# Kernel tuning notes

Measured on AMD Instinct MI355X. Metric: run time of the kernel, lower is better.

Reference implementation:

```python
import jax, jax.numpy as jnp
import numpy as np

BN_EPS = 1e-3  # keras BatchNormalization default epsilon


def conv1x1(x, w):
    # x: [N,C,H,W], w: [O,C] (1x1 conv, no bias)
    return jnp.einsum('nchw,oc->nohw', x, w)


def bn(x, gamma, beta, mean, var):
    # inference-mode batchnorm over channel axis 1
    scale = gamma / jnp.sqrt(var + BN_EPS)
    shift = beta - mean * scale
    return x * scale[None, :, None, None] + shift[None, :, None, None]


def fourier_unit(x, w, gamma, beta, mean, var):
    # x: [N,C,H,W] NCHW. 1D rfft over W (matches tf.signal.rfft), normalized by sqrt(W).
    N, C, H, W = x.shape
    norm = jnp.sqrt(jnp.float32(W))
    f = jnp.fft.rfft(x / norm, axis=-1)          # [N,C,H,Wf] complex64, Wf=W//2+1
    Wf = f.shape[-1]
    # interleave re/im per channel: [N,C,2,H,Wf] -> [N,2C,H,Wf]
    ff = jnp.stack([jnp.real(f), jnp.imag(f)], axis=2).reshape(N, 2 * C, H, Wf)
    y = jax.nn.relu(bn(conv1x1(ff, w), gamma, beta, mean, var))  # [N,2C,H,Wf]
    Co = y.shape[1] // 2
    y = y.reshape(N, Co, 2, H, Wf)
    c = jax.lax.complex(y[:, :, 0], y[:, :, 1])
    return jnp.fft.irfft(c, n=W, axis=-1) * norm  # [N,Co,H,W]


def setup_inputs() -> dict:
    key = jax.random.key(0)
    ks = jax.random.split(key, 20)
    N, H, W, Cin = 8, 128, 128, 256
    fmaps = 256
    half = fmaps // 2  # 128

    def nrm(k, shape, s=0.05):
        return jax.random.normal(k, shape, dtype=jnp.float32) * s

    def bn_params(k, c):
        k1, k2, k3, k4 = jax.random.split(k, 4)
        gamma = jax.random.uniform(k1, (c,), dtype=jnp.float32) + 0.5
        beta = nrm(k2, (c,), 0.1)
        mean = nrm(k3, (c,), 0.1)
        var = jax.random.uniform(k4, (c,), dtype=jnp.float32) + 0.5
        return gamma, beta, mean, var

    x = jax.random.normal(ks[0], (N, H, W, Cin), dtype=jnp.float32)
    w1 = nrm(ks[1], (half, Cin))
    g1, b1, m1, v1 = bn_params(ks[2], half)
    fu_w = nrm(ks[3], (2 * half, 2 * half))
    fu_g, fu_b, fu_m, fu_v = bn_params(ks[4], 2 * half)
    lfu_w = nrm(ks[5], (2 * half, 2 * half))
    lfu_g, lfu_b, lfu_m, lfu_v = bn_params(ks[6], 2 * half)
    w2 = nrm(ks[7], (fmaps, half))
    return {
        'x': x, 'w1': w1, 'g1': g1, 'b1': b1, 'm1': m1, 'v1': v1,
        'fu_w': fu_w, 'fu_g': fu_g, 'fu_b': fu_b, 'fu_m': fu_m, 'fu_v': fu_v,
        'lfu_w': lfu_w, 'lfu_g': lfu_g, 'lfu_b': lfu_b, 'lfu_m': lfu_m, 'lfu_v': lfu_v,
        'w2': w2,
    }


def reference(x, w1, g1, b1, m1, v1,
              fu_w, fu_g, fu_b, fu_m, fu_v,
              lfu_w, lfu_g, lfu_b, lfu_m, lfu_v,
              w2):
    # NHWC -> NCHW (stride=1, no downsample)
    x = jnp.transpose(x, (0, 3, 1, 2))
    x = jax.nn.relu(bn(conv1x1(x, w1), g1, b1, m1, v1))  # [N,half,H,W]
    out = fourier_unit(x, fu_w, fu_g, fu_b, fu_m, fu_v)
    # local fourier unit: take first C//4 channels, fold 2x2 spatial patches into channels
    C = x.shape[1]
    xs = x[:, :C // 4]
    xs = jnp.concatenate(jnp.split(xs, 2, axis=2), axis=1)  # split H
    xs = jnp.concatenate(jnp.split(xs, 2, axis=3), axis=1)  # split W -> [N,C,H/2,W/2]
    xs = fourier_unit(xs, lfu_w, lfu_g, lfu_b, lfu_m, lfu_v)
    xs = jnp.tile(xs, (1, 1, 2, 2))  # back to [N,C,H,W]
    out = conv1x1(x + out + xs, w2)  # [N,fmaps,H,W]
    return jnp.transpose(out, (0, 2, 3, 1))  # NCHW -> NHWC
```

## Files before the change

kernel.cpp:

```cpp
#include <hip/hip_runtime.h>
#include <math.h>

typedef __attribute__((ext_vector_type(8))) short short8;
typedef __attribute__((ext_vector_type(4))) float f32x4;

#define SW7b(r) (((r) & 7) << 4)
#define SW3b(r) (((r) & 3) << 4)

static __device__ __forceinline__ unsigned short f2b(float f){
  unsigned u = __float_as_uint(f);
  u = (u + 0x7FFFu + ((u >> 16) & 1u)) >> 16;
  return (unsigned short)u;
}
static __device__ __forceinline__ float b2f(unsigned short u){
  return __uint_as_float(((unsigned)u) << 16);
}
static __device__ __forceinline__ void gl16(const void* g, void* l) {
  __builtin_amdgcn_global_load_lds(
      (const __attribute__((address_space(1))) void*)g,
      (__attribute__((address_space(3))) void*)l, 16, 0, 0);
}

__global__ void k_wt(const float* __restrict__ w1, const float* __restrict__ fu_w,
                     const float* __restrict__ lfu_w, const float* __restrict__ w2,
                     const float* __restrict__ g1, const float* __restrict__ b1,
                     const float* __restrict__ m1, const float* __restrict__ v1,
                     const float* __restrict__ fg, const float* __restrict__ fb,
                     const float* __restrict__ fm, const float* __restrict__ fv,
                     const float* __restrict__ lg_, const float* __restrict__ lb_,
                     const float* __restrict__ lm_, const float* __restrict__ lv_,
                     unsigned short* __restrict__ w1b, unsigned short* __restrict__ fuwb,
                     unsigned short* __restrict__ lfuwb, unsigned short* __restrict__ w2b,
                     unsigned short* __restrict__ DFTf, unsigned short* __restrict__ IDFTf,
                     unsigned short* __restrict__ DFTl, unsigned short* __restrict__ IDFTl,
                     float* __restrict__ sc1, float* __restrict__ sh1,
                     float* __restrict__ scF, float* __restrict__ shF,
                     float* __restrict__ scL, float* __restrict__ shL) {
  int t = blockIdx.x * 256 + threadIdx.x;
  const float TPI = 6.283185307179586f;
  if (t < 32768) {
    { int co = t >> 8, k = t & 255; w1b[co * 256 + (k ^ ((co & 7) << 3))] = f2b(w1[t]); }
    { int co = t >> 7, k = t & 127; w2b[co * 128 + (k ^ ((co & 7) << 3))] = f2b(w2[t]); }
  }
  if (t < 65536) {
    int co = t >> 8, k = t & 255;
    fuwb[co * 256 + (k ^ ((co & 7) << 3))] = f2b(fu_w[t]);
    lfuwb[co * 256 + (k ^ ((co & 7) << 3))] = f2b(lfu_w[t]);
  }
  if (t < 18432) {
    int m = t >> 7, w = t & 127; float v = 0.f;
    if (m < 130) {
      int wf = m >> 1; int ph = (wf * w) & 127;
      float ang = TPI * (float)ph / 128.f;
      v = ((m & 1) ? -sinf(ang) : cosf(ang)) * 0.08838834764831845f;
    }
    DFTf[m * 128 + (w ^ ((m & 7) << 3))] = f2b(v);
  }
  if (t < 20480) {
    int m = t / 160, k2 = t % 160; float v = 0.f;
    if (k2 < 130) {
      int wf = k2 >> 1; float a = (wf == 0 || wf == 64) ? 1.f : 2.f;
      int ph = (wf * m) & 127;
      float ang = TPI * (float)ph / 128.f;
      v = ((k2 & 1) ? -a * sinf(ang) : a * cosf(ang)) * 0.08838834764831845f;
    }
    IDFTf[m * 160 + (k2 ^ ((m & 3) << 3))] = f2b(v);
  }
  if (t < 5120) {
    int m = t >> 6, w = t & 63; float v = 0.f;
    if (m < 66) {
      int wf = m >> 1; int ph = (wf * w) & 63;
      float ang = TPI * (float)ph / 64.f;
      v = ((m & 1) ? -sinf(ang) : cosf(ang)) * 0.125f;
    }
    DFTl[m * 64 + (w ^ ((m & 7) << 3))] = f2b(v);
  }
  if (t < 6144) {
    int m = t / 96, k2 = t % 96; float v = 0.f;
    if (k2 < 66) {
      int wf = k2 >> 1; float a = (wf == 0 || wf == 32) ? 1.f : 2.f;
      int ph = (wf * m) & 63;
      float ang = TPI * (float)ph / 64.f;
      v = ((k2 & 1) ? -a * sinf(ang) : a * cosf(ang)) * 0.125f;
    }
    IDFTl[m * 96 + (k2 ^ ((m & 3) << 3))] = f2b(v);
  }
  if (t < 128) { float s = g1[t] * rsqrtf(v1[t] + 1e-3f); sc1[t] = s; sh1[t] = b1[t] - m1[t] * s; }
  if (t < 256) { float s = fg[t] * rsqrtf(fv[t] + 1e-3f); scF[t] = s; shF[t] = fb[t] - fm[t] * s; }
  if (t < 256) { float s = lg_[t] * rsqrtf(lv_[t] + 1e-3f); scL[t] = s; shL[t] = lb_[t] - lm_[t] * s; }
}

__global__ __launch_bounds__(256) void k_conv1(const unsigned short* __restrict__ A,
                                               const float* __restrict__ x,
                                               unsigned short* __restrict__ X1c,
                                               const float* __restrict__ scp,
                                               const float* __restrict__ shp) {
  __shared__ __align__(16) char A_s[128 * 512];
  __shared__ __align__(16) char B_s[128 * 128];
  int t = threadIdx.x; int wid = t >> 6, l = t & 63;
  int wm = wid >> 1, wn = wid & 1;
  int m0 = wm * 64; int lr = l & 15, lg = l >> 4;
  size_t nh = blockIdx.x;
  const char* Ab = (const char*)A;
  const char* xrow = (const char*)(x + nh * 128 * 256);
  #pragma unroll
  for (int i = 0; i < 16; i++) { int g = i * 256 + t; gl16(Ab + g * 16, A_s + g * 16); }
  f32x4 acc[4][4];
  #pragma unroll
  for (int mt = 0; mt < 4; mt++)
    #pragma unroll
    for (int nt = 0; nt < 4; nt++) acc[mt][nt] = (f32x4){0.f, 0.f, 0.f, 0.f};
  for (int kk = 0; kk < 256; kk += 32) {
    #pragma unroll
    for (int i = 0; i < 4; i++) {
      int g = i * 256 + t; int w = g >> 3, o = g & 7;
      gl16(xrow + (size_t)w * 1024 + kk * 4 + ((o * 16) ^ SW7b(w)), B_s + g * 16);
    }
    __syncthreads();
    short8 af[4], bf[4];
    #pragma unroll
    for (int mt = 0; mt < 4; mt++) {
      int m = m0 + 16 * mt + lr;
      af[mt] = *(const short8*)(A_s + m * 512 + ((kk * 2 + lg * 16) ^ SW7b(m)));
    }
    #pragma unroll
    for (int nt = 0; nt < 4; nt++) {
      int w = wn * 64 + 16 * nt + lr;
      float4 f0 = *(const float4*)(B_s + w * 128 + ((lg * 32) ^ SW7b(w)));
      float4 f1 = *(const float4*)(B_s + w * 128 + ((lg * 32 + 16) ^ SW7b(w)));
      short8 bb;
      bb[0] = (short)f2b(f0.x); bb[1] = (short)f2b(f0.y);
      bb[2] = (short)f2b(f0.z); bb[3] = (short)f2b(f0.w);
      bb[4] = (short)f2b(f1.x); bb[5] = (short)f2b(f1.y);
      bb[6] = (short)f2b(f1.z); bb[7] = (short)f2b(f1.w);
      bf[nt] = bb;
    }
    #pragma unroll
    for (int mt = 0; mt < 4; mt++)
      #pragma unroll
      for (int nt = 0; nt < 4; nt++)
        acc[mt][nt] = __builtin_amdgcn_mfma_f32_16x16x32_bf16(af[mt], bf[nt], acc[mt][nt], 0, 0, 0);
    __syncthreads();
  }
  char* xout = (char*)X1c + nh * 32768;
  #pragma unroll
  for (int nt = 0; nt < 4; nt++) {
    int w = wn * 64 + 16 * nt + lr;
    #pragma unroll
    for (int mt = 0; mt < 4; mt++) {
      int rb = m0 + 16 * mt + lg * 4;
      float4 s4 = *(const float4*)&scp[rb];
      float4 h4 = *(const float4*)&shp[rb];
      f32x4 v = acc[mt][nt];
      *(unsigned short*)(xout + (rb + 0) * 256 + ((w * 2) ^ SW7b(rb + 0))) = f2b(fmaxf(v[0] * s4.x + h4.x, 0.f));
      *(unsigned short*)(xout + (rb + 1) * 256 + ((w * 2) ^ SW7b(rb + 1))) = f2b(fmaxf(v[1] * s4.y + h4.y, 0.f));
      *(unsigned short*)(xout + (rb + 2) * 256 + ((w * 2) ^ SW7b(rb + 2))) = f2b(fmaxf(v[2] * s4.z + h4.z, 0.f));
      *(unsigned short*)(xout + (rb + 3) * 256 + ((w * 2) ^ SW7b(rb + 3))) = f2b(fmaxf(v[3] * s4.w + h4.w, 0.f));
    }
  }
}

__global__ __launch_bounds__(256) void k_lfu(const unsigned short* __restrict__ DFTm,
                                             const unsigned short* __restrict__ lfuw,
                                             const unsigned short* __restrict__ IDFTm,
                                             const unsigned short* __restrict__ X1c,
                                             const float* __restrict__ scp,
                                             const float* __restrict__ shp,
                                             unsigned short* __restrict__ XSO) {
  __shared__ __align__(16) char SH[81920];
  char* M   = SH;
  char* Xs  = SH + 16384;
  char* FFl = SH + 32768;
  char* Yl  = SH + 57344;
  int t = threadIdx.x, wid = t >> 6, l = t & 63, lr = l & 15, lg = l >> 4;
  int b = blockIdx.x; int n = b >> 6, h2 = b & 63;
  {
    const char* src = (const char*)DFTm;
    #pragma unroll
    for (int i = 0; i < 3; i++) { int g = i * 256 + t; if (g < 640) gl16(src + g * 16, M + g * 16); }
    #pragma unroll
    for (int i = 0; i < 4; i++) {
      int g = i * 256 + t; int c2 = g >> 3, o = g & 7;
      int c0 = c2 & 31, hb = (c2 >> 5) & 1, wbq = (c2 >> 6) & 1;
      const char* s = (const char*)X1c +
          ((size_t)(n * 128 + hb * 64 + h2) * 128 + c0) * 256 + wbq * 128 + o * 16;
      gl16(s, Xs + g * 16);
    }
    #pragma unroll
    for (int i = 0; i < 8; i++) {
      int u = i * 256 + t;
      if (u < 1920) *(unsigned*)(FFl + 33 * 512 + u * 4) = 0u;
    }
  }
  __syncthreads();
  {
    f32x4 acc[5][2];
    #pragma unroll
    for (int mt = 0; mt < 5; mt++) { acc[mt][0] = (f32x4){0,0,0,0}; acc[mt][1] = (f32x4){0,0,0,0}; }
    for (int kk = 0; kk < 64; kk += 32) {
      int kb = kk * 2 + lg * 16;
      short8 bf[2];
      #pragma unroll
      for (int nt = 0; nt < 2; nt++) {
        int c2 = wid * 32 + 16 * nt + lr;
        bf[nt] = *(const short8*)(Xs + c2 * 128 + (kb ^ SW7b(c2)));
      }
      #pragma unroll
      for (int mt = 0; mt < 5; mt++) {
        int m = 16 * mt + lr;
        short8 af = *(const short8*)(M + m * 128 + (kb ^ SW7b(m)));
        #pragma unroll
        for (int nt = 0; nt < 2; nt++)
          acc[mt][nt] = __builtin_amdgcn_mfma_f32_16x16x32_bf16(af, bf[nt], acc[mt][nt], 0, 0, 0);
      }
    }
    #pragma unroll
    for (int nt = 0; nt < 2; nt++) {
      int c2 = wid * 32 + 16 * nt + lr;
      #pragma unroll
      for (int mt = 0; mt < 5; mt++) {
        int rb = 16 * mt + lg * 4;
        int wf0 = rb >> 1;
        f32x4 v = acc[mt][nt];
        if (wf0 < 33) {
          unsigned pk = (unsigned)f2b(v[0]) | ((unsigned)f2b(v[1]) << 16);
          *(unsigned*)(FFl + wf0 * 512 + ((4 * c2) ^ SW7b(wf0))) = pk;
        }
        if (wf0 + 1 < 33) {
          unsigned pk = (unsigned)f2b(v[2]) | ((unsigned)f2b(v[3]) << 16);
          *(unsigned*)(FFl + (wf0 + 1) * 512 + ((4 * c2) ^ SW7b(wf0 + 1))) = pk;
        }
      }
    }
  }
  __syncthreads();
  int wm2 = wid >> 1, wn2 = wid & 1;
  for (int ch = 0; ch < 8; ch++) {
    {
      const char* src = (const char*)lfuw + (size_t)ch * 16384;
      #pragma unroll
      for (int i = 0; i < 4; i++) { int g = i * 256 + t; gl16(src + g * 16, M + g * 16); }
    }
    __syncthreads();
    int NT = wn2 ? 1 : 2;
    f32x4 acc[2];
    acc[0] = (f32x4){0,0,0,0}; acc[1] = (f32x4){0,0,0,0};
    int lm = wm2 * 16 + lr;
    for (int kk = 0; kk < 256; kk += 32) {
      int kb = kk * 2 + lg * 16;
      short8 af = *(const short8*)(M + lm * 512 + (kb ^ SW7b(lm)));
      #pragma unroll
      for (int j = 0; j < 2; j++) {
        if (j < NT) {
          int wf = wn2 * 32 + 16 * j + lr;
          short8 bf = *(const short8*)(FFl + wf * 512 + (kb ^ SW7b(wf)));
          acc[j] = __builtin_amdgcn_mfma_f32_16x16x32_bf16(af, bf, acc[j], 0, 0, 0);
        }
      }
    }
    int co = ch * 32 + wm2 * 16 + lg * 4;
    float4 s4 = *(const float4*)&scp[co];
    float4 h4 = *(const float4*)&shp[co];
    int cc0 = co >> 1;
    #pragma unroll
    for (int j = 0; j < 2; j++) {
      if (j < NT) {
        int wf = wn2 * 32 + 16 * j + lr;
        f32x4 v = acc[j];
        float v0 = fmaxf(v[0] * s4.x + h4.x, 0.f);
        float v1 = fmaxf(v[1] * s4.y + h4.y, 0.f);
        float v2 = fmaxf(v[2] * s4.z + h4.z, 0.f);
        float v3 = fmaxf(v[3] * s4.w + h4.w, 0.f);
        unsigned p0 = (unsigned)f2b(v0) | ((unsigned)f2b(v1) << 16);
        unsigned p1 = (unsigned)f2b(v2) | ((unsigned)f2b(v3) << 16);
        *(unsigned*)(Yl + (cc0 + 0) * 192 + ((4 * wf) ^ SW3b(cc0 + 0))) = p0;
        *(unsigned*)(Yl + (cc0 + 1) * 192 + ((4 * wf) ^ SW3b(cc0 + 1))) = p1;
      }
    }
    __syncthreads();
  }
  {
    const char* src = (const char*)IDFTm;
    #pragma unroll
    for (int i = 0; i < 3; i++) { int g = i * 256 + t; gl16(src + g * 16, M + g * 16); }
  }
  __syncthreads();
  {
    f32x4 acc[8];
    #pragma unroll
    for (int nt = 0; nt < 8; nt++) acc[nt] = (f32x4){0,0,0,0};
    int w = wid * 16 + lr;
    for (int kk = 0; kk < 96; kk += 32) {
      int kb = kk * 2 + lg * 16;
      short8 af = *(const short8*)(M + w * 192 + (kb ^ SW3b(w)));
      #pragma unroll
      for (int nt = 0; nt < 8; nt++) {
        int cc = 16 * nt + lr;
        short8 bf = *(const short8*)(Yl + cc * 192 + (kb ^ SW3b(cc)));
        acc[nt] = __builtin_amdgcn_mfma_f32_16x16x32_bf16(af, bf, acc[nt], 0, 0, 0);
      }
    }
    int w0 = wid * 16 + lg * 4;
    #pragma unroll
    for (int nt = 0; nt < 8; nt++) {
      int cc = 16 * nt + lr;
      f32x4 v = acc[nt];
      ushort4 o;
      o.x = f2b(v[0]); o.y = f2b(v[1]); o.z = f2b(v[2]); o.w = f2b(v[3]);
      *(ushort4*)(XSO + (((size_t)n * 128 + cc) * 64 + h2) * 64 + w0) = o;
    }
  }
}

__global__ __launch_bounds__(1024, 4) void k_fu(const unsigned short* __restrict__ DFTm,
                                                const unsigned short* __restrict__ fuw,
                                                const unsigned short* __restrict__ IDFTm,
                                                const unsigned short* __restrict__ w2m,
                                                const unsigned short* __restrict__ X1c,
                                                const unsigned short* __restrict__ XSO,
                                                const float* __restrict__ scF,
                                                const float* __restrict__ shF,
                                                float* __restrict__ out) {
  __shared__ __align__(16) char SH[157696];
  char* M0 = SH;
  char* M1 = SH + 36864;
  char* FF = SH + 73728;
  char* Yb = SH + 114688;
  int t = threadIdx.x, wid = t >> 6, l = t & 63, lr = l & 15, lg = l >> 4;
  size_t nh = blockIdx.x;
  int n = (int)(nh >> 7), h = (int)(nh & 127);
  const char* xb = (const char*)X1c + nh * 32768;

  {
    const int nops = 36864 >> 4;
    #pragma unroll
    for (int i_ = 0; i_ < 3; i_++) {
      int g_ = i_ * 1024 + t;
      if (g_ < nops) gl16((const char*)DFTm + (size_t)g_ * 16, M0 + g_ * 16);
    }
    if (t < 1920) *(unsigned*)(FF + 65 * 512 + t * 4) = 0u;
  }
  __syncthreads();
  {
    #pragma unroll
    for (int i_ = 0; i_ < 2; i_++) {
      int g_ = i_ * 1024 + t;
      gl16((const char*)fuw + (size_t)g_ * 16, M1 + g_ * 16);
    }
    int wm1 = wid >> 3, wn1 = wid & 7;
    int c = wn1 * 16 + lr;
    short8 bf[4];
    #pragma unroll
    for (int ks = 0; ks < 4; ks++)
      bf[ks] = *(const short8*)(xb + c * 256 + ((ks * 64 + lg * 16) ^ SW7b(c)));
    f32x4 acc[5];
    #pragma unroll
    for (int mt = 0; mt < 5; mt++) acc[mt] = (f32x4){0,0,0,0};
    #pragma unroll
    for (int ks = 0; ks < 4; ks++) {
      int kb = ks * 64 + lg * 16;
      #pragma unroll
      for (int mt = 0; mt < 5; mt++) {
        int m = 16 * (wm1 * 4 + mt) + lr;
        short8 af = *(const short8*)(M0 + m * 256 + (kb ^ SW7b(m)));
        acc[mt] = __builtin_amdgcn_mfma_f32_16x16x32_bf16(af, bf[ks], acc[mt], 0, 0, 0);
      }
    }
    #pragma unroll
    for (int mt = 0; mt < 5; mt++) {
      int rb = 16 * (wm1 * 4 + mt) + lg * 4;
      int wf0 = rb >> 1;
      f32x4 v = acc[mt];
      if (wf0 < 65) {
        unsigned pk = (unsigned)f2b(v[0]) | ((unsigned)f2b(v[1]) << 16);
        *(unsigned*)(FF + wf0 * 512 + ((4 * c) ^ SW7b(wf0))) = pk;
      }
      if (wf0 + 1 < 65) {
        unsigned pk = (unsigned)f2b(v[2]) | ((unsigned)f2b(v[3]) << 16);
        *(unsigned*)(FF + (wf0 + 1) * 512 + ((4 * c) ^ SW7b(wf0 + 1))) = pk;
      }
    }
  }
  int mb2 = wid & 3, wn2 = wid >> 2;
  int mloc2 = mb2 * 16 + lr;
  #pragma unroll
  for (int ch = 0; ch < 4; ch++) {
    char* Mc = (ch & 1) ? M0 : M1;
    char* Mn = (ch & 1) ? M1 : M0;
    __syncthreads();
    if (ch < 3) {
      #pragma unroll
      for (int i_ = 0; i_ < 2; i_++) {
        int g_ = i_ * 1024 + t;
        gl16((const char*)fuw + (size_t)(ch + 1) * 32768 + (size_t)g_ * 16, Mn + g_ * 16);
      }
    } else {
      #pragma unroll
      for (int i_ = 0; i_ < 2; i_++) {
        int g_ = i_ * 1024 + t;
        if (g_ < 1280) gl16((const char*)IDFTm + (size_t)g_ * 16, Mn + g_ * 16);
      }
    }
    f32x4 acc[2];
    acc[0] = (f32x4){0,0,0,0}; acc[1] = (f32x4){0,0,0,0};
    int NJ = (wn2 == 0) ? 2 : 1;
    int j0 = wn2, j1 = 4;
    #pragma unroll
    for (int ks = 0; ks < 8; ks++) {
      int kb = ks * 64 + lg * 16;
      short8 af = *(const short8*)(Mc + mloc2 * 512 + (kb ^ SW7b(mloc2)));
      {
        int wf = j0 * 16 + lr;
        short8 b0 = *(const short8*)(FF + wf * 512 + (kb ^ SW7b(wf)));
        acc[0] = __builtin_amdgcn_mfma_f32_16x16x32_bf16(af, b0, acc[0], 0, 0, 0);
      }
      if (NJ == 2) {
        int wf = j1 * 16 + lr;
        short8 b1 = *(const short8*)(FF + wf * 512 + (kb ^ SW7b(wf)));
        acc[1] = __builtin_amdgcn_mfma_f32_16x16x32_bf16(af, b1, acc[1], 0, 0, 0);
      }
    }
    int co = ch * 64 + mb2 * 16 + lg * 4;
    float4 s4 = *(const float4*)&scF[co];
    float4 h4 = *(const float4*)&shF[co];
    int cc0 = co >> 1;
    #pragma unroll
    for (int jj = 0; jj < 2; jj++) {
      if (jj < NJ) {
        int wf = (jj == 0 ? j0 : j1) * 16 + lr;
        f32x4 v = acc[jj];
        float v0 = fmaxf(v[0] * s4.x + h4.x, 0.f);
        float v1 = fmaxf(v[1] * s4.y + h4.y, 0.f);
        float v2 = fmaxf(v[2] * s4.z + h4.z, 0.f);
        float v3 = fmaxf(v[3] * s4.w + h4.w, 0.f);
        unsigned p0 = (unsigned)f2b(v0) | ((unsigned)f2b(v1) << 16);
        unsigned p1 = (unsigned)f2b(v2) | ((unsigned)f2b(v3) << 16);
        *(unsigned*)(Yb + (size_t)(cc0 + 0) * 336 + 4 * wf) = p0;
        *(unsigned*)(Yb + (size_t)(cc0 + 1) * 336 + 4 * wf) = p1;
      }
    }
  }
  int mb3 = wid & 3, wn3 = wid >> 2;
  #pragma unroll
  for (int ck = 0; ck < 2; ck++) {
    char* Mc = ck ? M0 : M1;
    __syncthreads();
    if (ck == 0) {
      #pragma unroll
      for (int i_ = 0; i_ < 2; i_++) {
        int g_ = i_ * 1024 + t;
        if (g_ < 1280) gl16((const char*)IDFTm + 20480 + (size_t)g_ * 16, M0 + g_ * 16);
      }
    } else {
      #pragma unroll
      for (int i_ = 0; i_ < 2; i_++) {
        int g_ = i_ * 1024 + t;
        gl16((const char*)w2m + (size_t)g_ * 16, M1 + g_ * 16);
      }
    }
    int mloc = mb3 * 16 + lr;
    int w0 = ck * 64 + mb3 * 16 + lg * 4;
    ushort4 rx[2], rs[2];
    #pragma unroll
    for (int jj = 0; jj < 2; jj++) {
      int cc = (wn3 + jj * 4) * 16 + lr;
      rx[jj] = *(const ushort4*)(xb + cc * 256 + ((w0 * 2) ^ SW7b(cc)));
      rs[jj] = *(const ushort4*)(XSO + (((size_t)n * 128 + cc) * 64 + (h & 63)) * 64 + (w0 & 63));
    }
    f32x4 acc[2];
    acc[0] = (f32x4){0,0,0,0}; acc[1] = (f32x4){0,0,0,0};
    #pragma unroll
    for (int ks = 0; ks < 5; ks++) {
      int kb = ks * 64 + lg * 16;
      short8 af = *(const short8*)(Mc + mloc * 320 + (kb ^ SW3b(mloc)));
      #pragma unroll
      for (int jj = 0; jj < 2; jj++) {
        int cc = (wn3 + jj * 4) * 16 + lr;
        short8 bf = *(const short8*)(Yb + (size_t)cc * 336 + kb);
        acc[jj] = __builtin_amdgcn_mfma_f32_16x16x32_bf16(af, bf, acc[jj], 0, 0, 0);
      }
    }
    #pragma unroll
    for (int jj = 0; jj < 2; jj++) {
      int cc = (wn3 + jj * 4) * 16 + lr;
      f32x4 v = acc[jj];
      float f0 = v[0] + b2f(rx[jj].x) + b2f(rs[jj].x);
      float f1 = v[1] + b2f(rx[jj].y) + b2f(rs[jj].y);
      float f2_ = v[2] + b2f(rx[jj].z) + b2f(rs[jj].z);
      float f3 = v[3] + b2f(rx[jj].w) + b2f(rs[jj].w);
      *(unsigned short*)(FF + (w0 + 0) * 256 + ((cc * 2) ^ SW7b(w0 + 0))) = f2b(f0);
      *(unsigned short*)(FF + (w0 + 1) * 256 + ((cc * 2) ^ SW7b(w0 + 1))) = f2b(f1);
      *(unsigned short*)(FF + (w0 + 2) * 256 + ((cc * 2) ^ SW7b(w0 + 2))) = f2b(f2_);
      *(unsigned short*)(FF + (w0 + 3) * 256 + ((cc * 2) ^ SW7b(w0 + 3))) = f2b(f3);
    }
  }
  int mb4 = wid & 7, wn4 = wid >> 3;
  int mloc4 = mb4 * 16 + lr;
  #pragma unroll
  for (int ck = 0; ck < 2; ck++) {
    char* Mc = ck ? M0 : M1;
    __syncthreads();
    if (ck == 0) {
      #pragma unroll
      for (int i_ = 0; i_ < 2; i_++) {
        int g_ = i_ * 1024 + t;
        gl16((const char*)w2m + 32768 + (size_t)g_ * 16, M0 + g_ * 16);
      }
    }
    f32x4 acc[4];
    #pragma unroll
    for (int nt = 0; nt < 4; nt++) acc[nt] = (f32x4){0,0,0,0};
    #pragma unroll
    for (int ks = 0; ks < 4; ks++) {
      int kb = ks * 64 + lg * 16;
      short8 af = *(const short8*)(Mc + mloc4 * 256 + (kb ^ SW7b(mloc4)));
      #pragma unroll
      for (int nt = 0; nt < 4; nt++) {
        int w = (wn4 * 4 + nt) * 16 + lr;
        short8 bf = *(const short8*)(FF + w * 256 + (kb ^ SW7b(w)));
        acc[nt] = __builtin_amdgcn_mfma_f32_16x16x32_bf16(af, bf, acc[nt], 0, 0, 0);
      }
    }
    int co2 = ck * 128 + mb4 * 16 + lg * 4;
    #pragma unroll
    for (int nt = 0; nt < 4; nt++) {
      int w = (wn4 * 4 + nt) * 16 + lr;
      f32x4 v = acc[nt];
      float4 o; o.x = v[0]; o.y = v[1]; o.z = v[2]; o.w = v[3];
      *(float4*)(out + (nh * 128 + w) * 256 + co2) = o;
    }
  }
}

extern "C" void kernel_launch(void* const* d_in, const int* in_sizes, int n_in,
                              void* d_out, int out_size, void* d_ws, size_t ws_size,
                              hipStream_t stream) {
  const float* x     = (const float*)d_in[0];
  const float* w1    = (const float*)d_in[1];
  const float* g1    = (const float*)d_in[2];
  const float* b1    = (const float*)d_in[3];
  const float* m1    = (const float*)d_in[4];
  const float* v1    = (const float*)d_in[5];
  const float* fu_w  = (const float*)d_in[6];
  const float* fu_g  = (const float*)d_in[7];
  const float* fu_b  = (const float*)d_in[8];
  const float* fu_m  = (const float*)d_in[9];
  const float* fu_v  = (const float*)d_in[10];
  const float* lfu_w = (const float*)d_in[11];
  const float* lfu_g = (const float*)d_in[12];
  const float* lfu_b = (const float*)d_in[13];
  const float* lfu_m = (const float*)d_in[14];
  const float* lfu_v = (const float*)d_in[15];
  const float* w2    = (const float*)d_in[16];
  float* out = (float*)d_out;

  char* p = (char*)d_ws;
  unsigned short* X1c = (unsigned short*)p; p += 33554432;
  unsigned short* XSO = (unsigned short*)p; p += 8388608;
  unsigned short* w1b   = (unsigned short*)p; p += 65536;
  unsigned short* fuwb  = (unsigned short*)p; p += 131072;
  unsigned short* lfuwb = (unsigned short*)p; p += 131072;
  unsigned short* w2b   = (unsigned short*)p; p += 65536;
  unsigned short* DFTf  = (unsigned short*)p; p += 36864;
  unsigned short* IDFTf = (unsigned short*)p; p += 40960;
  unsigned short* DFTl  = (unsigned short*)p; p += 10240;
  unsigned short* IDFTl = (unsigned short*)p; p += 12288;
  float* sc1 = (float*)p; p += 512;
  float* sh1 = (float*)p; p += 512;
  float* scF = (float*)p; p += 1024;
  float* shF = (float*)p; p += 1024;
  float* scL = (float*)p; p += 1024;
  float* shL = (float*)p; p += 1024;

  k_wt<<<dim3(256), dim3(256), 0, stream>>>(w1, fu_w, lfu_w, w2, g1, b1, m1, v1,
                                            fu_g, fu_b, fu_m, fu_v, lfu_g, lfu_b, lfu_m, lfu_v,
                                            w1b, fuwb, lfuwb, w2b, DFTf, IDFTf, DFTl, IDFTl,
                                            sc1, sh1, scF, shF, scL, shL);
  k_conv1<<<dim3(1024), dim3(256), 0, stream>>>(w1b, x, X1c, sc1, sh1);
  k_lfu<<<dim3(512), dim3(256), 0, stream>>>(DFTl, lfuwb, IDFTl, X1c, scL, shL, XSO);
  k_fu<<<dim3(1024), dim3(1024), 0, stream>>>(DFTf, fuwb, IDFTf, w2b, X1c, XSO, scF, shF, out);
}
```

Baseline: 163.9 us.

## Double-buffer conv1 input tiles, two rows per block; repad IDFT matrix

```diff
diff --git a/kernel.cpp b/kernel.cpp
--- a/kernel.cpp
+++ b/kernel.cpp
@@ -56,15 +56,15 @@
     }
     DFTf[m * 128 + (w ^ ((m & 7) << 3))] = f2b(v);
   }
-  if (t < 20480) {
-    int m = t / 160, k2 = t % 160; float v = 0.f;
+  if (t < 24576) {
+    int m = t / 192, k2 = t % 192; float v = 0.f;
     if (k2 < 130) {
       int wf = k2 >> 1; float a = (wf == 0 || wf == 64) ? 1.f : 2.f;
       int ph = (wf * m) & 127;
       float ang = TPI * (float)ph / 128.f;
       v = ((k2 & 1) ? -a * sinf(ang) : a * cosf(ang)) * 0.08838834764831845f;
     }
-    IDFTf[m * 160 + (k2 ^ ((m & 3) << 3))] = f2b(v);
+    IDFTf[m * 192 + (k2 ^ ((m & 7) << 3))] = f2b(v);
   }
   if (t < 5120) {
     int m = t >> 6, w = t & 63; float v = 0.f;
@@ -90,33 +90,44 @@
   if (t < 256) { float s = lg_[t] * rsqrtf(lv_[t] + 1e-3f); scL[t] = s; shL[t] = lb_[t] - lm_[t] * s; }
 }
 
-__global__ __launch_bounds__(256) void k_conv1(const unsigned short* __restrict__ A,
+__global__ __launch_bounds__(512) void k_conv1(const unsigned short* __restrict__ A,
                                                const float* __restrict__ x,
                                                unsigned short* __restrict__ X1c,
                                                const float* __restrict__ scp,
                                                const float* __restrict__ shp) {
   __shared__ __align__(16) char A_s[128 * 512];
-  __shared__ __align__(16) char B_s[128 * 128];
+  __shared__ __align__(16) char B_s[2][32768];
   int t = threadIdx.x; int wid = t >> 6, l = t & 63;
-  int wm = wid >> 1, wn = wid & 1;
-  int m0 = wm * 64; int lr = l & 15, lg = l >> 4;
-  size_t nh = blockIdx.x;
+  int wm = wid >> 2, wn = wid & 3;
+  int m0 = wm * 64, n0 = wn * 64;
+  int lr = l & 15, lg = l >> 4;
+  size_t nh0 = (size_t)blockIdx.x * 2;
   const char* Ab = (const char*)A;
-  const char* xrow = (const char*)(x + nh * 128 * 256);
-  #pragma unroll
-  for (int i = 0; i < 16; i++) { int g = i * 256 + t; gl16(Ab + g * 16, A_s + g * 16); }
+  const char* xrow = (const char*)(x + nh0 * 32768);
+  #pragma unroll
+  for (int i = 0; i < 8; i++) { int g = i * 512 + t; gl16(Ab + g * 16, A_s + g * 16); }
+  #pragma unroll
+  for (int i = 0; i < 4; i++) {
+    int g = i * 512 + t; int w = g >> 3, o = g & 7;
+    gl16(xrow + (size_t)w * 1024 + ((o * 16) ^ SW7b(w)), B_s[0] + g * 16);
+  }
   f32x4 acc[4][4];
   #pragma unroll
   for (int mt = 0; mt < 4; mt++)
     #pragma unroll
     for (int nt = 0; nt < 4; nt++) acc[mt][nt] = (f32x4){0.f, 0.f, 0.f, 0.f};
-  for (int kk = 0; kk < 256; kk += 32) {
-    #pragma unroll
-    for (int i = 0; i < 4; i++) {
-      int g = i * 256 + t; int w = g >> 3, o = g & 7;
-      gl16(xrow + (size_t)w * 1024 + kk * 4 + ((o * 16) ^ SW7b(w)), B_s + g * 16);
-    }
-    __syncthreads();
+  __syncthreads();
+  for (int it = 0; it < 8; it++) {
+    int kk = it * 32;
+    if (it < 7) {
+      #pragma unroll
+      for (int i = 0; i < 4; i++) {
+        int g = i * 512 + t; int w = g >> 3, o = g & 7;
+        gl16(xrow + (size_t)w * 1024 + (kk + 32) * 4 + ((o * 16) ^ SW7b(w)),
+             B_s[(it + 1) & 1] + g * 16);
+      }
+    }
+    const char* Bc = B_s[it & 1];
     short8 af[4], bf[4];
     #pragma unroll
     for (int mt = 0; mt < 4; mt++) {
@@ -125,9 +136,9 @@
     }
     #pragma unroll
     for (int nt = 0; nt < 4; nt++) {
-      int w = wn * 64 + 16 * nt + lr;
-      float4 f0 = *(const float4*)(B_s + w * 128 + ((lg * 32) ^ SW7b(w)));
-      float4 f1 = *(const float4*)(B_s + w * 128 + ((lg * 32 + 16) ^ SW7b(w)));
+      int w = n0 + 16 * nt + lr;
+      float4 f0 = *(const float4*)(Bc + w * 128 + ((lg * 32) ^ SW7b(w)));
+      float4 f1 = *(const float4*)(Bc + w * 128 + ((lg * 32 + 16) ^ SW7b(w)));
       short8 bb;
       bb[0] = (short)f2b(f0.x); bb[1] = (short)f2b(f0.y);
       bb[2] = (short)f2b(f0.z); bb[3] = (short)f2b(f0.w);
@@ -142,10 +153,11 @@
         acc[mt][nt] = __builtin_amdgcn_mfma_f32_16x16x32_bf16(af[mt], bf[nt], acc[mt][nt], 0, 0, 0);
     __syncthreads();
   }
-  char* xout = (char*)X1c + nh * 32768;
   #pragma unroll
   for (int nt = 0; nt < 4; nt++) {
-    int w = wn * 64 + 16 * nt + lr;
+    int wcol = n0 + 16 * nt + lr;
+    char* xout = (char*)X1c + (nh0 + (wcol >> 7)) * 32768;
+    int w = wcol & 127;
     #pragma unroll
     for (int mt = 0; mt < 4; mt++) {
       int rb = m0 + 16 * mt + lg * 4;
@@ -330,6 +342,8 @@
   size_t nh = blockIdx.x;
   int n = (int)(nh >> 7), h = (int)(nh & 127);
   const char* xb = (const char*)X1c + nh * 32768;
+  char* Xs = M0 + 0;
+  (void)Xs;
 
   {
     const int nops = 36864 >> 4;
@@ -398,7 +412,7 @@
       #pragma unroll
       for (int i_ = 0; i_ < 2; i_++) {
         int g_ = i_ * 1024 + t;
-        if (g_ < 1280) gl16((const char*)IDFTm + (size_t)g_ * 16, Mn + g_ * 16);
+        if (g_ < 1536) gl16((const char*)IDFTm + (size_t)g_ * 16, Mn + g_ * 16);
       }
     }
     f32x4 acc[2];
@@ -449,7 +463,7 @@
       #pragma unroll
       for (int i_ = 0; i_ < 2; i_++) {
         int g_ = i_ * 1024 + t;
-        if (g_ < 1280) gl16((const char*)IDFTm + 20480 + (size_t)g_ * 16, M0 + g_ * 16);
+        if (g_ < 1536) gl16((const char*)IDFTm + 24576 + (size_t)g_ * 16, M0 + g_ * 16);
       }
     } else {
       #pragma unroll
@@ -472,7 +486,7 @@
     #pragma unroll
     for (int ks = 0; ks < 5; ks++) {
       int kb = ks * 64 + lg * 16;
-      short8 af = *(const short8*)(Mc + mloc * 320 + (kb ^ SW3b(mloc)));
+      short8 af = *(const short8*)(Mc + mloc * 384 + (kb ^ SW7b(mloc)));
       #pragma unroll
       for (int jj = 0; jj < 2; jj++) {
         int cc = (wn3 + jj * 4) * 16 + lr;
@@ -562,7 +576,7 @@
   unsigned short* lfuwb = (unsigned short*)p; p += 131072;
   unsigned short* w2b   = (unsigned short*)p; p += 65536;
   unsigned short* DFTf  = (unsigned short*)p; p += 36864;
-  unsigned short* IDFTf = (unsigned short*)p; p += 40960;
+  unsigned short* IDFTf = (unsigned short*)p; p += 49152;
   unsigned short* DFTl  = (unsigned short*)p; p += 10240;
   unsigned short* IDFTl = (unsigned short*)p; p += 12288;
   float* sc1 = (float*)p; p += 512;
@@ -576,7 +590,7 @@
                                             fu_g, fu_b, fu_m, fu_v, lfu_g, lfu_b, lfu_m, lfu_v,
                                             w1b, fuwb, lfuwb, w2b, DFTf, IDFTf, DFTl, IDFTl,
                                             sc1, sh1, scF, shF, scL, shL);
-  k_conv1<<<dim3(1024), dim3(256), 0, stream>>>(w1b, x, X1c, sc1, sh1);
+  k_conv1<<<dim3(512), dim3(512), 0, stream>>>(w1b, x, X1c, sc1, sh1);
   k_lfu<<<dim3(512), dim3(256), 0, stream>>>(DFTl, lfuwb, IDFTl, X1c, scL, shL, XSO);
   k_fu<<<dim3(1024), dim3(1024), 0, stream>>>(DFTf, fuwb, IDFTf, w2b, X1c, XSO, scF, shF, out);
 }
```

New measurement: 152.3 us. 7.1% less time.
